# Optimization experiments

Hardware: AMD Instinct MI355X
Metric: run time of the kernel (lower is better)

Reference implementation:

```python
import jax, jax.numpy as jnp
import numpy as np

LOCAL_RADIUS = 5


def setup_inputs() -> dict:
    key = jax.random.key(0)
    k1, k2, k3 = jax.random.split(key, 3)
    B, K, C, H = 4, 4096, 256, 128
    x = jax.random.normal(k1, (B, K, C), dtype=jnp.float32)
    W1 = jax.random.normal(k2, (C, H), dtype=jnp.float32) * (1.0 / np.sqrt(C))
    b1 = jnp.zeros((H,), dtype=jnp.float32)
    W2 = jax.random.normal(k3, (H, 1), dtype=jnp.float32) * (1.0 / np.sqrt(H))
    b2 = jnp.zeros((1,), dtype=jnp.float32)
    return {"x": x, "W1": W1, "b1": b1, "W2": W2, "b2": b2}


def reference(x, W1, b1, W2, b2):
    # x: [B, k, C]. The MLP score for column j is independent of the row i,
    # so compute it once per token instead of per (i, window) as in the torch loop.
    B, k, C = x.shape
    s = (jnp.tanh(x @ W1 + b1) @ W2 + b2)[..., 0]  # [B, k]
    idx = jnp.arange(k)
    band = (jnp.abs(idx[:, None] - idx[None, :]) <= LOCAL_RADIUS)  # [k, k]
    # Outside the band the original leaves scores at 0.0 (not -inf), so
    # out-of-window positions still contribute exp(0)=1 to the softmax.
    scores = jnp.where(band[None, :, :], s[:, None, :], jnp.float32(0.0))  # [B, k, k]
    weights = jax.nn.softmax(scores, axis=-1)  # [B, k, k]
    weighted = jnp.einsum('bij,bjc->bic', weights, x)  # [B, k, C]
    return weighted, weights
```

## Files before the change

### kernel.cpp

```cpp
#include <hip/hip_runtime.h>
#include <math.h>

#define B_ 4
#define K_ 4096
#define C_ 256
#define H_ 128
#define RAD 5
#define NB (2 * RAD + 1)
#define PSTRIDE 12
#define TROWS 16

typedef float floatx4 __attribute__((ext_vector_type(4)));


__global__ __launch_bounds__(128) void score_kernel(
    const float* __restrict__ x, const float* __restrict__ W1,
    const float* __restrict__ b1, const float* __restrict__ W2,
    const float* __restrict__ b2, float* __restrict__ s_out)
{
    const int tid = threadIdx.x;
    const int t0 = blockIdx.x * 8;
    const float* xr[8];
    #pragma unroll
    for (int t = 0; t < 8; ++t) xr[t] = x + (size_t)(t0 + t) * C_;

    float acc[8];
    float binit = b1[tid];
    #pragma unroll
    for (int t = 0; t < 8; ++t) acc[t] = binit;

    for (int c = 0; c < C_; c += 4) {
        float w0 = W1[(c + 0) * H_ + tid];
        float w1 = W1[(c + 1) * H_ + tid];
        float w2 = W1[(c + 2) * H_ + tid];
        float w3 = W1[(c + 3) * H_ + tid];
        #pragma unroll
        for (int t = 0; t < 8; ++t) {
            floatx4 xv = *(const floatx4*)&xr[t][c];
            acc[t] = fmaf(xv.x, w0, acc[t]);
            acc[t] = fmaf(xv.y, w1, acc[t]);
            acc[t] = fmaf(xv.z, w2, acc[t]);
            acc[t] = fmaf(xv.w, w3, acc[t]);
        }
    }

    __shared__ float red[2][8];
    float w2v = W2[tid];
    #pragma unroll
    for (int t = 0; t < 8; ++t) {
        float p = tanhf(acc[t]) * w2v;
        #pragma unroll
        for (int off = 32; off > 0; off >>= 1) p += __shfl_down(p, off);
        if ((tid & 63) == 0) red[tid >> 6][t] = p;
    }
    __syncthreads();
    if (tid < 8) s_out[t0 + tid] = red[0][tid] + red[1][tid] + b2[0];
}

__global__ __launch_bounds__(256) void colsum_partial(
    const float* __restrict__ x, float* __restrict__ partial)
{
    const int tid = threadIdx.x;
    const int blk = blockIdx.x;
    const float* base = x + (size_t)blk * 32 * C_ + tid;
    float a0 = 0.f, a1 = 0.f, a2 = 0.f, a3 = 0.f;
    #pragma unroll
    for (int kk = 0; kk < 32; kk += 4) {
        a0 += base[(size_t)(kk + 0) * C_];
        a1 += base[(size_t)(kk + 1) * C_];
        a2 += base[(size_t)(kk + 2) * C_];
        a3 += base[(size_t)(kk + 3) * C_];
    }
    partial[(size_t)blk * C_ + tid] = (a0 + a1) + (a2 + a3);
}

__global__ __launch_bounds__(1024) void colsum_final(
    const float* __restrict__ partial, float* __restrict__ Ssum)
{
    const int c = threadIdx.x & 255;
    const int g = threadIdx.x >> 8;
    const int b = blockIdx.x;
    __shared__ float red[4][C_];
    float acc = 0.f;
    const float* pb = partial + ((size_t)b * 128 + g * 32) * C_ + c;
    #pragma unroll 4
    for (int ch = 0; ch < 32; ++ch) acc += pb[(size_t)ch * C_];
    red[g][c] = acc;
    __syncthreads();
    if (g == 0) Ssum[b * C_ + c] = red[0][c] + red[1][c] + red[2][c] + red[3][c];
}

__global__ __launch_bounds__(256) void params_kernel(
    const float* __restrict__ s, float* __restrict__ params)
{
    const int row = blockIdx.x * 256 + threadIdx.x;
    const int b = row >> 12;
    const int i = row & (K_ - 1);
    const int j0 = max(0, i - RAD), j1 = min(K_ - 1, i + RAD);
    const int nb = j1 - j0 + 1;
    const float* srow = s + b * K_;

    float sv[NB];
    float m = 0.f;
    #pragma unroll
    for (int jj = 0; jj < NB; ++jj) {
        float v = (jj < nb) ? srow[j0 + jj] : 0.f;
        sv[jj] = v;
        if (jj < nb) m = fmaxf(m, v);
    }
    float e0 = expf(-m);
    float D = (float)(K_ - nb) * e0;
    float* pp = params + (size_t)row * PSTRIDE;
    #pragma unroll
    for (int jj = 0; jj < NB; ++jj) {
        float e = expf(sv[jj] - m);
        if (jj < nb) D += e;
        sv[jj] = e;
    }
    float inv = 1.0f / D;
    #pragma unroll
    for (int jj = 0; jj < NB; ++jj) pp[jj] = sv[jj] * inv;
    pp[11] = e0 * inv;
}

__global__ __launch_bounds__(256) void store16_kernel(
    const float* __restrict__ x, const float* __restrict__ params,
    const float* __restrict__ Ssum, float* __restrict__ out)
{
    const int tid = threadIdx.x;
    const int blk = blockIdx.x;
    const int b  = blk >> 8;
    const int i0 = (blk & 255) * TROWS;

    const int j0t = max(0, i0 - RAD);
    const int j1t = min(K_ - 1, i0 + TROWS - 1 + RAD);
    const int ntok = j1t - j0t + 1;

    __shared__ float xs[TROWS + 2 * RAD][C_];
    __shared__ float prm[TROWS][PSTRIDE];

    if (tid < TROWS * PSTRIDE)
        ((float*)prm)[tid] = params[(size_t)(b * K_ + i0) * PSTRIDE + tid];
    const floatx4* xsrc = (const floatx4*)(x + ((size_t)b * K_ + j0t) * C_);
    floatx4* xdst = (floatx4*)&xs[0][0];
    for (int f = tid; f < ntok * (C_ / 4); f += 256) xdst[f] = xsrc[f];
    __syncthreads();

    const float sc = Ssum[b * C_ + tid];
    #pragma unroll
    for (int r = 0; r < TROWS; ++r) {
        const int i = i0 + r;
        const int j0 = max(0, i - RAD), j1 = min(K_ - 1, i + RAD);
        const float wo = prm[r][11];
        float acc = wo * sc;
        for (int j = j0; j <= j1; ++j)
            acc = fmaf(prm[r][j - j0] - wo, xs[j - j0t][tid], acc);
        out[((size_t)b * K_ + i) * C_ + tid] = acc;
    }

    float* wbase = out + (size_t)B_ * K_ * C_ + ((size_t)b * K_ + i0) * K_;
    #pragma unroll
    for (int r = 0; r < TROWS; ++r) {
        const int i = i0 + r;
        const int j0 = max(0, i - RAD), j1 = min(K_ - 1, i + RAD);
        const float wo = prm[r][11];
        floatx4* wrow4 = (floatx4*)(wbase + (size_t)r * K_);
        #pragma unroll
        for (int q = 0; q < 4; ++q) {
            const int f = tid + 256 * q;
            const int jb = f * 4;
            floatx4 v = { wo, wo, wo, wo };
            if (jb + 3 >= j0 && jb <= j1) {
                if (jb + 0 >= j0 && jb + 0 <= j1) v.x = prm[r][jb + 0 - j0];
                if (jb + 1 >= j0 && jb + 1 <= j1) v.y = prm[r][jb + 1 - j0];
                if (jb + 2 >= j0 && jb + 2 <= j1) v.z = prm[r][jb + 2 - j0];
                if (jb + 3 >= j0 && jb + 3 <= j1) v.w = prm[r][jb + 3 - j0];
            }
            wrow4[f] = v;
        }
    }
}

extern "C" void kernel_launch(void* const* d_in, const int* in_sizes, int n_in,
                              void* d_out, int out_size, void* d_ws, size_t ws_size,
                              hipStream_t stream) {
    const float* x  = (const float*)d_in[0];
    const float* W1 = (const float*)d_in[1];
    const float* b1 = (const float*)d_in[2];
    const float* W2 = (const float*)d_in[3];
    const float* b2 = (const float*)d_in[4];
    float* out = (float*)d_out;

    float* ws      = (float*)d_ws;
    float* s       = ws;
    float* Ssum    = ws + 16384;
    float* partial = ws + 17408;
    float* params  = ws + 148480;

    score_kernel  <<<B_ * K_ / 8,      128,  0, stream>>>(x, W1, b1, W2, b2, s);
    colsum_partial<<<B_ * 128,         256,  0, stream>>>(x, partial);
    colsum_final  <<<B_,               1024, 0, stream>>>(partial, Ssum);
    params_kernel <<<B_ * K_ / 256,    256,  0, stream>>>(s, params);
    store16_kernel<<<B_ * K_ / TROWS,  256,  0, stream>>>(x, params, Ssum, out);
}
```

Measured before the change: 383.9 us.

## Split weighted-sum and dense weight-row fill into separate kernels

The fused store kernel, which computed the banded weighted sum and also wrote the full dense weights rows, is split into two kernels. weighted_kernel now handles 8 rows per block with x staged in shared memory. A new wfill_kernel streams the 256 MB weights matrix, reading the band parameters straight from global memory. The off-band weight moves from params slot 11 into its own array. The aim is to let the large write-bound fill run at full occupancy without the shared-memory staging overhead, at the cost of one more launch and some repeated parameter reads.

```diff
diff --git a/kernel.cpp b/kernel.cpp
--- a/kernel.cpp
+++ b/kernel.cpp
@@ -8,7 +8,8 @@
 #define RAD 5
 #define NB (2 * RAD + 1)
 #define PSTRIDE 12
-#define TROWS 16
+#define WROWS 8
+#define FROWS 8
 
 typedef float floatx4 __attribute__((ext_vector_type(4)));
 
@@ -91,7 +92,8 @@
 }
 
 __global__ __launch_bounds__(256) void params_kernel(
-    const float* __restrict__ s, float* __restrict__ params)
+    const float* __restrict__ s, float* __restrict__ params,
+    float* __restrict__ woff_arr)
 {
     const int row = blockIdx.x * 256 + threadIdx.x;
     const int b = row >> 12;
@@ -120,27 +122,31 @@
     float inv = 1.0f / D;
     #pragma unroll
     for (int jj = 0; jj < NB; ++jj) pp[jj] = sv[jj] * inv;
-    pp[11] = e0 * inv;
-}
-
-__global__ __launch_bounds__(256) void store16_kernel(
+    woff_arr[row] = e0 * inv;
+}
+
+__global__ __launch_bounds__(256) void weighted_kernel(
     const float* __restrict__ x, const float* __restrict__ params,
-    const float* __restrict__ Ssum, float* __restrict__ out)
+    const float* __restrict__ woff_arr, const float* __restrict__ Ssum,
+    float* __restrict__ out)
 {
     const int tid = threadIdx.x;
     const int blk = blockIdx.x;
-    const int b  = blk >> 8;
-    const int i0 = (blk & 255) * TROWS;
+    const int b  = blk >> 9;
+    const int i0 = (blk & 511) * WROWS;
 
     const int j0t = max(0, i0 - RAD);
-    const int j1t = min(K_ - 1, i0 + TROWS - 1 + RAD);
+    const int j1t = min(K_ - 1, i0 + WROWS - 1 + RAD);
     const int ntok = j1t - j0t + 1;
 
-    __shared__ float xs[TROWS + 2 * RAD][C_];
-    __shared__ float prm[TROWS][PSTRIDE];
-
-    if (tid < TROWS * PSTRIDE)
+    __shared__ float xs[WROWS + 2 * RAD][C_];
+    __shared__ float prm[WROWS][PSTRIDE];
+    __shared__ float wo_s[WROWS];
+
+    if (tid < WROWS * PSTRIDE)
         ((float*)prm)[tid] = params[(size_t)(b * K_ + i0) * PSTRIDE + tid];
+    if (tid >= 128 && tid < 128 + WROWS)
+        wo_s[tid - 128] = woff_arr[b * K_ + i0 + (tid - 128)];
     const floatx4* xsrc = (const floatx4*)(x + ((size_t)b * K_ + j0t) * C_);
     floatx4* xdst = (floatx4*)&xs[0][0];
     for (int f = tid; f < ntok * (C_ / 4); f += 256) xdst[f] = xsrc[f];
@@ -148,35 +154,45 @@
 
     const float sc = Ssum[b * C_ + tid];
     #pragma unroll
-    for (int r = 0; r < TROWS; ++r) {
+    for (int r = 0; r < WROWS; ++r) {
         const int i = i0 + r;
         const int j0 = max(0, i - RAD), j1 = min(K_ - 1, i + RAD);
-        const float wo = prm[r][11];
+        const float wo = wo_s[r];
         float acc = wo * sc;
         for (int j = j0; j <= j1; ++j)
             acc = fmaf(prm[r][j - j0] - wo, xs[j - j0t][tid], acc);
         out[((size_t)b * K_ + i) * C_ + tid] = acc;
     }
-
-    float* wbase = out + (size_t)B_ * K_ * C_ + ((size_t)b * K_ + i0) * K_;
-    #pragma unroll
-    for (int r = 0; r < TROWS; ++r) {
-        const int i = i0 + r;
+}
+
+__global__ __launch_bounds__(256) void wfill_kernel(
+    const float* __restrict__ params, const float* __restrict__ woff_arr,
+    float* __restrict__ out)
+{
+    const int tid = threadIdx.x;
+    const int r0 = blockIdx.x * FROWS;
+    floatx4* wbase = (floatx4*)(out + (size_t)B_ * K_ * C_) + (size_t)r0 * (K_ / 4);
+
+    #pragma unroll
+    for (int m = 0; m < FROWS; ++m) {
+        const int rr = r0 + m;
+        const int i = rr & (K_ - 1);
         const int j0 = max(0, i - RAD), j1 = min(K_ - 1, i + RAD);
-        const float wo = prm[r][11];
-        floatx4* wrow4 = (floatx4*)(wbase + (size_t)r * K_);
+        const float wo = woff_arr[rr];
+        floatx4* wrow = wbase + (size_t)m * (K_ / 4);
         #pragma unroll
         for (int q = 0; q < 4; ++q) {
-            const int f = tid + 256 * q;
+            const int f = q * 256 + tid;
             const int jb = f * 4;
             floatx4 v = { wo, wo, wo, wo };
             if (jb + 3 >= j0 && jb <= j1) {
-                if (jb + 0 >= j0 && jb + 0 <= j1) v.x = prm[r][jb + 0 - j0];
-                if (jb + 1 >= j0 && jb + 1 <= j1) v.y = prm[r][jb + 1 - j0];
-                if (jb + 2 >= j0 && jb + 2 <= j1) v.z = prm[r][jb + 2 - j0];
-                if (jb + 3 >= j0 && jb + 3 <= j1) v.w = prm[r][jb + 3 - j0];
+                const float* pp = params + (size_t)rr * PSTRIDE;
+                if (jb + 0 >= j0 && jb + 0 <= j1) v.x = pp[jb + 0 - j0];
+                if (jb + 1 >= j0 && jb + 1 <= j1) v.y = pp[jb + 1 - j0];
+                if (jb + 2 >= j0 && jb + 2 <= j1) v.z = pp[jb + 2 - j0];
+                if (jb + 3 >= j0 && jb + 3 <= j1) v.w = pp[jb + 3 - j0];
             }
-            wrow4[f] = v;
+            wrow[f] = v;
         }
     }
 }
@@ -191,15 +207,17 @@
     const float* b2 = (const float*)d_in[4];
     float* out = (float*)d_out;
 
-    float* ws      = (float*)d_ws;
-    float* s       = ws;
-    float* Ssum    = ws + 16384;
-    float* partial = ws + 17408;
-    float* params  = ws + 148480;
-
-    score_kernel  <<<B_ * K_ / 8,      128,  0, stream>>>(x, W1, b1, W2, b2, s);
-    colsum_partial<<<B_ * 128,         256,  0, stream>>>(x, partial);
-    colsum_final  <<<B_,               1024, 0, stream>>>(partial, Ssum);
-    params_kernel <<<B_ * K_ / 256,    256,  0, stream>>>(s, params);
-    store16_kernel<<<B_ * K_ / TROWS,  256,  0, stream>>>(x, params, Ssum, out);
-}
+    float* ws       = (float*)d_ws;
+    float* s        = ws;
+    float* Ssum     = ws + 16384;
+    float* partial  = ws + 17408;
+    float* params   = ws + 148480;
+    float* woff_arr = ws + 345088;
+
+    score_kernel   <<<B_ * K_ / 8,     128,  0, stream>>>(x, W1, b1, W2, b2, s);
+    colsum_partial <<<B_ * 128,        256,  0, stream>>>(x, partial);
+    colsum_final   <<<B_,              1024, 0, stream>>>(partial, Ssum);
+    params_kernel  <<<B_ * K_ / 256,   256,  0, stream>>>(s, params, woff_arr);
+    weighted_kernel<<<B_ * K_ / WROWS, 256,  0, stream>>>(x, params, woff_arr, Ssum, out);
+    wfill_kernel   <<<B_ * K_ / FROWS, 256,  0, stream>>>(params, woff_arr, out);
+}
```

Measured after the change: 387.9 us. No clear change (+1.0%).
